# Kernel optimization log

Measured on AMD Instinct MI355X. Metric: run time of the kernel, lower is better.

Reference implementation:

```python
import jax, jax.numpy as jnp
import numpy as np

B, P, F, H, C, D = 512, 32, 16, 4, 32, 128   # graphs, nodes/graph, node feat, heads, head_dim, hidden
N = B * P
E_DIM = 5

def _lin(k, o, i):
    return jax.random.normal(k, (o, i)) * (1.0 / np.sqrt(i))

def setup_inputs():
    key = jax.random.key(0)
    ks = jax.random.split(key, 32)
    # fully-connected directed edges (no self loops) within each graph
    a = np.repeat(np.arange(P), P); b = np.tile(np.arange(P), P)
    m = a != b; a, b = a[m], b[m]
    off = (np.arange(B) * P)[:, None]
    src = (a[None, :] + off).reshape(-1); dst = (b[None, :] + off).reshape(-1)
    edge_index = jnp.asarray(np.stack([src, dst]), dtype=jnp.int32)
    E = src.size
    x = jax.random.normal(ks[0], (N, F))
    edge_attr = jax.random.normal(ks[1], (E, E_DIM))
    z = jnp.zeros
    return dict(
        x=x, edge_index=edge_index, edge_attr=edge_attr,
        W1l=_lin(ks[2], D, F), b1l=z(D), W1r=_lin(ks[3], D, F), b1r=z(D),
        W1e=_lin(ks[4], D, E_DIM), att1=jax.random.normal(ks[5], (1, H, C)) * 0.1, bias1=z(D),
        W2l=_lin(ks[6], D, D), b2l=z(D), W2r=_lin(ks[7], D, D), b2r=z(D),
        W2e=_lin(ks[8], D, E_DIM), att2=jax.random.normal(ks[9], (1, H, C)) * 0.1, bias2=z(D),
        Wc1=_lin(ks[10], D, D), bc1=z(D), Wc2=_lin(ks[11], 1, D), bc2=z(1),
        Ws1=_lin(ks[12], D, D), bs1=z(D), Ws2=_lin(ks[13], 1, D), bs2=z(1),
        Wn1=_lin(ks[14], D, D), bn1=z(D), Wn2=_lin(ks[15], 1, D), bn2=z(1),
    )

def _gatv2(x, src, dst, edge_attr, Wl, bl, Wr, br, We, att, bias):
    # PyG GATv2Conv, concat=True, heads=H, out_channels=C, edge_dim=E_DIM, add_self_loops=False
    E = src.shape[0]
    xl = x @ Wl.T + bl                                   # [N, H*C] messages (source side)
    xr = x @ Wr.T + br                                   # [N, H*C] destination side
    e = (xl[src] + xr[dst] + edge_attr @ We.T).reshape(E, H, C)
    g = jax.nn.leaky_relu(e, 0.2)
    score = jnp.sum(g * att, axis=-1)                    # [E, H]
    smax = jax.ops.segment_max(score, dst, num_segments=N)
    ex = jnp.exp(score - smax[dst])
    denom = jax.ops.segment_sum(ex, dst, num_segments=N)
    alpha = ex / (denom[dst] + 1e-16)                    # segment softmax over in-edges of dst
    msg = xl[src].reshape(E, H, C) * alpha[..., None]
    return jax.ops.segment_sum(msg, dst, num_segments=N).reshape(N, H * C) + bias

def _mlp(h, W1, b1, W2, b2):
    return jax.nn.relu(h @ W1.T + b1) @ W2.T + b2

def reference(x, edge_index, edge_attr, W1l, b1l, W1r, b1r, W1e, att1, bias1,
              W2l, b2l, W2r, b2r, W2e, att2, bias2,
              Wc1, bc1, Wc2, bc2, Ws1, bs1, Ws2, bs2, Wn1, bn1, Wn2, bn2):
    src, dst = edge_index[0], edge_index[1]
    h = _gatv2(x, src, dst, edge_attr, W1l, b1l, W1r, b1r, W1e, att1, bias1)
    hb = h.reshape(B, P, D)
    h = (hb - hb.mean(axis=1, keepdims=True)).reshape(N, D)   # MeanSubtractionNorm per graph
    h = jax.nn.relu(h)
    h = jax.nn.relu(_gatv2(h, src, dst, edge_attr, W2l, b2l, W2r, b2r, W2e, att2, bias2))
    g = h.reshape(B, P, D).mean(axis=1)                       # global_mean_pool (equal-size graphs)
    value = _mlp(g, Wc1, bc1, Wc2, bc2)                       # critic        [B, 1]
    src_logits = _mlp(h, Ws1, bs1, Ws2, bs2).reshape(B, P)    # source_actor, dense per graph
    noop = _mlp(g, Wn1, bn1, Wn2, bn2)                        # noop_actor    [B, 1]
    return jnp.concatenate([value, noop, src_logits], axis=1) # [B, P+2]
```

## Files before the change

kernel.cpp:

```cpp
#include <hip/hip_runtime.h>

#define PP    32
#define FF    16
#define HH    4
#define CC    32
#define DD    128
#define EDIM  5
#define EPG   992
#define NB    512

template <int CTRL>
__device__ __forceinline__ float dpp_add(float v) {
    int t = __builtin_amdgcn_update_dpp(0, __builtin_bit_cast(int, v), CTRL, 0xF, 0xF, true);
    return v + __builtin_bit_cast(float, t);
}
__device__ __forceinline__ float red64(float v) {
    v = dpp_add<0x111>(v);
    v = dpp_add<0x112>(v);
    v = dpp_add<0x114>(v);
    v = dpp_add<0x118>(v);
    v = dpp_add<0x142>(v);
    v = dpp_add<0x143>(v);
    return v;
}
__device__ __forceinline__ float redquad(float v) {
    v = dpp_add<0xB1>(v);
    v = dpp_add<0x4E>(v);
    return v;
}

__device__ __forceinline__ void attention(const float* __restrict__ eattr,
                                          const float* __restrict__ We, const float* __restrict__ att,
                                          const float* __restrict__ bias,
                                          const float* __restrict__ sMsg, const float* __restrict__ sDst,
                                          float* __restrict__ sS, float* __restrict__ sOut,
                                          int tid, long eBase, bool relu)
{
    {
        const int s  = tid >> 4;
        const int ch0 = (tid & 15) * 8;
        float we[40], at[8], xl[8];
#pragma unroll
        for (int q = 0; q < 10; ++q)
            *(float4*)(we + q * 4) = *(const float4*)(We + ch0 * EDIM + q * 4);
        *(float4*)(at)     = *(const float4*)(att + ch0);
        *(float4*)(at + 4) = *(const float4*)(att + ch0 + 4);
        *(float4*)(xl)     = *(const float4*)(sMsg + s * DD + ch0);
        *(float4*)(xl + 4) = *(const float4*)(sMsg + s * DD + ch0 + 4);

        for (int d = 0; d < PP; ++d) {
            int jj = d - (d > s);
            if (jj > 30) jj = 30;
            const float* ea = eattr + (eBase + s * 31 + jj) * EDIM;
            const float e0 = ea[0], e1 = ea[1], e2 = ea[2], e3 = ea[3], e4 = ea[4];
            float xr[8];
            *(float4*)(xr)     = *(const float4*)(sDst + d * DD + ch0);
            *(float4*)(xr + 4) = *(const float4*)(sDst + d * DD + ch0 + 4);
            float acc0 = 0.f, acc1 = 0.f;
#pragma unroll
            for (int c = 0; c < 8; ++c) {
                float v = xl[c] + xr[c];
                const float* w = we + c * EDIM;
                v = fmaf(w[0], e0, v); v = fmaf(w[1], e1, v); v = fmaf(w[2], e2, v);
                v = fmaf(w[3], e3, v); v = fmaf(w[4], e4, v);
                v = fmaf(0.4f, fabsf(v), 0.6f * v);
                if (c & 1) acc1 = fmaf(v, at[c], acc1);
                else       acc0 = fmaf(v, at[c], acc0);
            }
            const float r = redquad(acc0 + acc1);
            if ((tid & 3) == 0)
                sS[s * DD + d * HH + ((tid >> 2) & 3)] = r;
        }
    }
    __syncthreads();
    if (tid < PP * HH) {
        const int d = tid >> 2;
        float mx = -3.4e38f;
#pragma unroll
        for (int s = 0; s < PP; ++s) if (s != d) mx = fmaxf(mx, sS[s * DD + tid]);
        float sum = 0.f;
#pragma unroll
        for (int s = 0; s < PP; ++s) {
            if (s != d) { float ex = __expf(sS[s * DD + tid] - mx); sS[s * DD + tid] = ex; sum += ex; }
        }
        const float inv = 1.f / (sum + 1e-16f);
#pragma unroll
        for (int s = 0; s < PP; ++s)
            sS[s * DD + tid] = (s == d) ? 0.f : sS[s * DD + tid] * inv;
    }
    __syncthreads();
    {
        const int d = tid >> 4, sub = tid & 15;
#pragma unroll
        for (int half = 0; half < 2; ++half) {
            const int ch4 = half * 16 + sub;
            const int idx = d * HH + (ch4 >> 3);
            const float* bp = bias + ch4 * 4;
            float4 acc = make_float4(bp[0], bp[1], bp[2], bp[3]);
#pragma unroll
            for (int s = 0; s < PP; ++s) {
                const float a = sS[s * DD + idx];
                const float4 xv = *(const float4*)(sMsg + s * DD + ch4 * 4);
                acc.x = fmaf(a, xv.x, acc.x);
                acc.y = fmaf(a, xv.y, acc.y);
                acc.z = fmaf(a, xv.z, acc.z);
                acc.w = fmaf(a, xv.w, acc.w);
            }
            if (relu) {
                acc.x = fmaxf(acc.x, 0.f); acc.y = fmaxf(acc.y, 0.f);
                acc.z = fmaxf(acc.z, 0.f); acc.w = fmaxf(acc.w, 0.f);
            }
            *(float4*)(sOut + d * DD + ch4 * 4) = acc;
        }
    }
}

extern "C" __global__ void __launch_bounds__(512, 4)
planetwars_gnn_kernel(const float* __restrict__ x, const float* __restrict__ eattr,
                      const float* __restrict__ W1l, const float* __restrict__ b1l,
                      const float* __restrict__ W1r, const float* __restrict__ b1r,
                      const float* __restrict__ W1e, const float* __restrict__ att1, const float* __restrict__ bias1,
                      const float* __restrict__ W2l, const float* __restrict__ b2l,
                      const float* __restrict__ W2r, const float* __restrict__ b2r,
                      const float* __restrict__ W2e, const float* __restrict__ att2, const float* __restrict__ bias2,
                      const float* __restrict__ Wc1, const float* __restrict__ bc1,
                      const float* __restrict__ Wc2, const float* __restrict__ bc2,
                      const float* __restrict__ Ws1, const float* __restrict__ bs1,
                      const float* __restrict__ Ws2, const float* __restrict__ bs2,
                      const float* __restrict__ Wn1, const float* __restrict__ bn1,
                      const float* __restrict__ Wn2, const float* __restrict__ bn2,
                      float* __restrict__ out)
{
    __shared__ __align__(16) float sA[PP * DD];
    __shared__ __align__(16) float sB[PP * DD];
    __shared__ __align__(16) float sH[PP * DD];
    __shared__ __align__(16) float sU[PP * DD];

    const int tid = threadIdx.x;
    const int g = blockIdx.x;
    const long eBase = (long)g * EPG;

    sU[tid] = x[g * PP * FF + tid];
    __syncthreads();

    {
        const int j = tid & 127, d0 = (tid >> 7) * 8;
        float wl[16], wr[16];
#pragma unroll
        for (int q = 0; q < 4; ++q) {
            *(float4*)(wl + q * 4) = *(const float4*)(W1l + j * FF + q * 4);
            *(float4*)(wr + q * 4) = *(const float4*)(W1r + j * FF + q * 4);
        }
        const float bl = b1l[j], br = b1r[j];
#pragma unroll
        for (int i = 0; i < 8; ++i) {
            const float* xr = sU + (d0 + i) * FF;
            float al = bl, ar = br;
#pragma unroll
            for (int k = 0; k < FF; ++k) {
                const float xv = xr[k];
                al = fmaf(wl[k], xv, al);
                ar = fmaf(wr[k], xv, ar);
            }
            sA[(d0 + i) * DD + j] = al;
            sB[(d0 + i) * DD + j] = ar;
        }
    }
    __syncthreads();

    attention(eattr, W1e, att1, bias1, sA, sB, sU, sH, tid, eBase, false);
    __syncthreads();

    if (tid < DD) {
        float s = 0.f;
#pragma unroll
        for (int d = 0; d < PP; ++d) s += sH[d * DD + tid];
        const float mn = s * (1.0f / 32.0f);
#pragma unroll
        for (int d = 0; d < PP; ++d)
            sH[d * DD + tid] = fmaxf(sH[d * DD + tid] - mn, 0.f);
    }
    __syncthreads();

    {
        const int jj = tid & 63, d0 = (tid >> 6) * 4;
        float accL0[4], accL1[4], accR0[4], accR1[4];
        const float bl0 = b2l[jj], bl1 = b2l[jj + 64];
        const float br0 = b2r[jj], br1 = b2r[jj + 64];
#pragma unroll
        for (int i = 0; i < 4; ++i) { accL0[i] = bl0; accL1[i] = bl1; accR0[i] = br0; accR1[i] = br1; }
        const float* WL0 = W2l + jj * DD;
        const float* WL1 = W2l + (jj + 64) * DD;
        const float* WR0 = W2r + jj * DD;
        const float* WR1 = W2r + (jj + 64) * DD;
        for (int k8 = 0; k8 < 16; ++k8) {
            const float4 l00 = *(const float4*)(WL0 + k8 * 8), l01 = *(const float4*)(WL0 + k8 * 8 + 4);
            const float4 l10 = *(const float4*)(WL1 + k8 * 8), l11 = *(const float4*)(WL1 + k8 * 8 + 4);
            const float4 r00 = *(const float4*)(WR0 + k8 * 8), r01 = *(const float4*)(WR0 + k8 * 8 + 4);
            const float4 r10 = *(const float4*)(WR1 + k8 * 8), r11 = *(const float4*)(WR1 + k8 * 8 + 4);
#pragma unroll
            for (int i = 0; i < 4; ++i) {
                const float4 a0 = *(const float4*)(sH + (d0 + i) * DD + k8 * 8);
                const float4 a1 = *(const float4*)(sH + (d0 + i) * DD + k8 * 8 + 4);
                accL0[i] = fmaf(l00.x, a0.x, accL0[i]); accL0[i] = fmaf(l00.y, a0.y, accL0[i]);
                accL0[i] = fmaf(l00.z, a0.z, accL0[i]); accL0[i] = fmaf(l00.w, a0.w, accL0[i]);
                accL0[i] = fmaf(l01.x, a1.x, accL0[i]); accL0[i] = fmaf(l01.y, a1.y, accL0[i]);
                accL0[i] = fmaf(l01.z, a1.z, accL0[i]); accL0[i] = fmaf(l01.w, a1.w, accL0[i]);
                accL1[i] = fmaf(l10.x, a0.x, accL1[i]); accL1[i] = fmaf(l10.y, a0.y, accL1[i]);
                accL1[i] = fmaf(l10.z, a0.z, accL1[i]); accL1[i] = fmaf(l10.w, a0.w, accL1[i]);
                accL1[i] = fmaf(l11.x, a1.x, accL1[i]); accL1[i] = fmaf(l11.y, a1.y, accL1[i]);
                accL1[i] = fmaf(l11.z, a1.z, accL1[i]); accL1[i] = fmaf(l11.w, a1.w, accL1[i]);
                accR0[i] = fmaf(r00.x, a0.x, accR0[i]); accR0[i] = fmaf(r00.y, a0.y, accR0[i]);
                accR0[i] = fmaf(r00.z, a0.z, accR0[i]); accR0[i] = fmaf(r00.w, a0.w, accR0[i]);
                accR0[i] = fmaf(r01.x, a1.x, accR0[i]); accR0[i] = fmaf(r01.y, a1.y, accR0[i]);
                accR0[i] = fmaf(r01.z, a1.z, accR0[i]); accR0[i] = fmaf(r01.w, a1.w, accR0[i]);
                accR1[i] = fmaf(r10.x, a0.x, accR1[i]); accR1[i] = fmaf(r10.y, a0.y, accR1[i]);
                accR1[i] = fmaf(r10.z, a0.z, accR1[i]); accR1[i] = fmaf(r10.w, a0.w, accR1[i]);
                accR1[i] = fmaf(r11.x, a1.x, accR1[i]); accR1[i] = fmaf(r11.y, a1.y, accR1[i]);
                accR1[i] = fmaf(r11.z, a1.z, accR1[i]); accR1[i] = fmaf(r11.w, a1.w, accR1[i]);
            }
        }
#pragma unroll
        for (int i = 0; i < 4; ++i) {
            sA[(d0 + i) * DD + jj]      = accL0[i];
            sA[(d0 + i) * DD + jj + 64] = accL1[i];
            sB[(d0 + i) * DD + jj]      = accR0[i];
            sB[(d0 + i) * DD + jj + 64] = accR1[i];
        }
    }
    __syncthreads();

    attention(eattr, W2e, att2, bias2, sA, sB, sU, sH, tid, eBase, true);
    __syncthreads();

    if (tid < DD) {
        float s = 0.f;
#pragma unroll
        for (int d = 0; d < PP; ++d) s += sH[d * DD + tid];
        sU[tid] = s * (1.0f / 32.0f);
    }
    __syncthreads();

    {
        const int jj = tid & 63, d0 = (tid >> 6) * 4;
        const float b0 = bs1[jj], b1 = bs1[jj + 64];
        float acc0[4], acc1[4];
#pragma unroll
        for (int i = 0; i < 4; ++i) { acc0[i] = b0; acc1[i] = b1; }
        const float* W0 = Ws1 + jj * DD;
        const float* W1 = Ws1 + (jj + 64) * DD;
        for (int k8 = 0; k8 < 16; ++k8) {
            const float4 w00 = *(const float4*)(W0 + k8 * 8), w01 = *(const float4*)(W0 + k8 * 8 + 4);
            const float4 w10 = *(const float4*)(W1 + k8 * 8), w11 = *(const float4*)(W1 + k8 * 8 + 4);
#pragma unroll
            for (int i = 0; i < 4; ++i) {
                const float4 a0 = *(const float4*)(sH + (d0 + i) * DD + k8 * 8);
                const float4 a1 = *(const float4*)(sH + (d0 + i) * DD + k8 * 8 + 4);
                acc0[i] = fmaf(w00.x, a0.x, acc0[i]); acc0[i] = fmaf(w00.y, a0.y, acc0[i]);
                acc0[i] = fmaf(w00.z, a0.z, acc0[i]); acc0[i] = fmaf(w00.w, a0.w, acc0[i]);
                acc0[i] = fmaf(w01.x, a1.x, acc0[i]); acc0[i] = fmaf(w01.y, a1.y, acc0[i]);
                acc0[i] = fmaf(w01.z, a1.z, acc0[i]); acc0[i] = fmaf(w01.w, a1.w, acc0[i]);
                acc1[i] = fmaf(w10.x, a0.x, acc1[i]); acc1[i] = fmaf(w10.y, a0.y, acc1[i]);
                acc1[i] = fmaf(w10.z, a0.z, acc1[i]); acc1[i] = fmaf(w10.w, a0.w, acc1[i]);
                acc1[i] = fmaf(w11.x, a1.x, acc1[i]); acc1[i] = fmaf(w11.y, a1.y, acc1[i]);
                acc1[i] = fmaf(w11.z, a1.z, acc1[i]); acc1[i] = fmaf(w11.w, a1.w, acc1[i]);
            }
        }
        const float ws2a = Ws2[jj], ws2b = Ws2[jj + 64];
        const float bias2s = bs2[0];
#pragma unroll
        for (int i = 0; i < 4; ++i) {
            const float t = fmaf(fmaxf(acc0[i], 0.f), ws2a, fmaxf(acc1[i], 0.f) * ws2b);
            const float r = red64(t);
            if ((tid & 63) == 63) out[g * 34 + 2 + d0 + i] = r + bias2s;
        }
    }

    if (tid < 128) {
        const int w = tid >> 6, j = tid & 63;
        const float* Wa = (w ? Wn1 : Wc1);
        const float* ba = (w ? bn1 : bc1);
        const float* Wb = (w ? Wn2 : Wc2);
        const float  bb = (w ? bn2 : bc2)[0];
        float h0 = ba[j], h1 = ba[j + 64];
        const float* R0 = Wa + j * DD;
        const float* R1 = Wa + (j + 64) * DD;
#pragma unroll
        for (int k8 = 0; k8 < 16; ++k8) {
            const float4 g0 = *(const float4*)(sU + k8 * 8);
            const float4 g1 = *(const float4*)(sU + k8 * 8 + 4);
            const float4 p00 = *(const float4*)(R0 + k8 * 8), p01 = *(const float4*)(R0 + k8 * 8 + 4);
            const float4 p10 = *(const float4*)(R1 + k8 * 8), p11 = *(const float4*)(R1 + k8 * 8 + 4);
            h0 = fmaf(p00.x, g0.x, h0); h0 = fmaf(p00.y, g0.y, h0);
            h0 = fmaf(p00.z, g0.z, h0); h0 = fmaf(p00.w, g0.w, h0);
            h0 = fmaf(p01.x, g1.x, h0); h0 = fmaf(p01.y, g1.y, h0);
            h0 = fmaf(p01.z, g1.z, h0); h0 = fmaf(p01.w, g1.w, h0);
            h1 = fmaf(p10.x, g0.x, h1); h1 = fmaf(p10.y, g0.y, h1);
            h1 = fmaf(p10.z, g0.z, h1); h1 = fmaf(p10.w, g0.w, h1);
            h1 = fmaf(p11.x, g1.x, h1); h1 = fmaf(p11.y, g1.y, h1);
            h1 = fmaf(p11.z, g1.z, h1); h1 = fmaf(p11.w, g1.w, h1);
        }
        const float t = fmaf(fmaxf(h0, 0.f), Wb[j], fmaxf(h1, 0.f) * Wb[j + 64]);
        const float r = red64(t);
        if (j == 63) out[g * 34 + w] = r + bb;
    }
}

extern "C" void kernel_launch(void* const* d_in, const int* in_sizes, int n_in,
                              void* d_out, int out_size, void* d_ws, size_t ws_size,
                              hipStream_t stream)
{
    (void)in_sizes; (void)n_in; (void)d_ws; (void)ws_size; (void)out_size;
    planetwars_gnn_kernel<<<dim3(NB), dim3(512), 0, stream>>>(
        (const float*)d_in[0], (const float*)d_in[2],
        (const float*)d_in[3], (const float*)d_in[4], (const float*)d_in[5], (const float*)d_in[6],
        (const float*)d_in[7], (const float*)d_in[8], (const float*)d_in[9],
        (const float*)d_in[10], (const float*)d_in[11], (const float*)d_in[12], (const float*)d_in[13],
        (const float*)d_in[14], (const float*)d_in[15], (const float*)d_in[16],
        (const float*)d_in[17], (const float*)d_in[18], (const float*)d_in[19], (const float*)d_in[20],
        (const float*)d_in[21], (const float*)d_in[22], (const float*)d_in[23], (const float*)d_in[24],
        (const float*)d_in[25], (const float*)d_in[26], (const float*)d_in[27], (const float*)d_in[28],
        (float*)d_out);
}
```

Baseline: 252.5 us.

## Double block size to 1024 threads and halve per-thread work in all stages

```diff
diff --git a/kernel.cpp b/kernel.cpp
--- a/kernel.cpp
+++ b/kernel.cpp
@@ -23,9 +23,10 @@
     v = dpp_add<0x143>(v);
     return v;
 }
-__device__ __forceinline__ float redquad(float v) {
-    v = dpp_add<0xB1>(v);
-    v = dpp_add<0x4E>(v);
+__device__ __forceinline__ float red8(float v) {
+    v = dpp_add<0x111>(v);
+    v = dpp_add<0x112>(v);
+    v = dpp_add<0x114>(v);
     return v;
 }
 
@@ -37,39 +38,58 @@
                                           int tid, long eBase, bool relu)
 {
     {
-        const int s  = tid >> 4;
-        const int ch0 = (tid & 15) * 8;
-        float we[40], at[8], xl[8];
-#pragma unroll
-        for (int q = 0; q < 10; ++q)
-            *(float4*)(we + q * 4) = *(const float4*)(We + ch0 * EDIM + q * 4);
-        *(float4*)(at)     = *(const float4*)(att + ch0);
-        *(float4*)(at + 4) = *(const float4*)(att + ch0 + 4);
-        *(float4*)(xl)     = *(const float4*)(sMsg + s * DD + ch0);
-        *(float4*)(xl + 4) = *(const float4*)(sMsg + s * DD + ch0 + 4);
+        const int s = tid >> 5;
+        const int q = tid & 31;
+        float we[4][EDIM], at[4], xl[4];
+        {
+            const float* wp = We + q * 20;
+#pragma unroll
+            for (int c = 0; c < 4; ++c)
+#pragma unroll
+                for (int k = 0; k < EDIM; ++k) we[c][k] = wp[c * EDIM + k];
+        }
+        *(float4*)at = *(const float4*)(att + q * 4);
+        *(float4*)xl = *(const float4*)(sMsg + s * DD + q * 4);
+        const float* eaBase = eattr + (eBase + (long)s * 31) * EDIM;
 
         for (int d = 0; d < PP; ++d) {
             int jj = d - (d > s);
             if (jj > 30) jj = 30;
-            const float* ea = eattr + (eBase + s * 31 + jj) * EDIM;
+            const float* ea = eaBase + jj * EDIM;
             const float e0 = ea[0], e1 = ea[1], e2 = ea[2], e3 = ea[3], e4 = ea[4];
-            float xr[8];
-            *(float4*)(xr)     = *(const float4*)(sDst + d * DD + ch0);
-            *(float4*)(xr + 4) = *(const float4*)(sDst + d * DD + ch0 + 4);
-            float acc0 = 0.f, acc1 = 0.f;
-#pragma unroll
-            for (int c = 0; c < 8; ++c) {
-                float v = xl[c] + xr[c];
-                const float* w = we + c * EDIM;
-                v = fmaf(w[0], e0, v); v = fmaf(w[1], e1, v); v = fmaf(w[2], e2, v);
-                v = fmaf(w[3], e3, v); v = fmaf(w[4], e4, v);
+            const float4 xr = *(const float4*)(sDst + d * DD + q * 4);
+            float acc;
+            {
+                float v = xl[0] + xr.x;
+                v = fmaf(we[0][0], e0, v); v = fmaf(we[0][1], e1, v); v = fmaf(we[0][2], e2, v);
+                v = fmaf(we[0][3], e3, v); v = fmaf(we[0][4], e4, v);
                 v = fmaf(0.4f, fabsf(v), 0.6f * v);
-                if (c & 1) acc1 = fmaf(v, at[c], acc1);
-                else       acc0 = fmaf(v, at[c], acc0);
-            }
-            const float r = redquad(acc0 + acc1);
-            if ((tid & 3) == 0)
-                sS[s * DD + d * HH + ((tid >> 2) & 3)] = r;
+                acc = v * at[0];
+            }
+            {
+                float v = xl[1] + xr.y;
+                v = fmaf(we[1][0], e0, v); v = fmaf(we[1][1], e1, v); v = fmaf(we[1][2], e2, v);
+                v = fmaf(we[1][3], e3, v); v = fmaf(we[1][4], e4, v);
+                v = fmaf(0.4f, fabsf(v), 0.6f * v);
+                acc = fmaf(v, at[1], acc);
+            }
+            {
+                float v = xl[2] + xr.z;
+                v = fmaf(we[2][0], e0, v); v = fmaf(we[2][1], e1, v); v = fmaf(we[2][2], e2, v);
+                v = fmaf(we[2][3], e3, v); v = fmaf(we[2][4], e4, v);
+                v = fmaf(0.4f, fabsf(v), 0.6f * v);
+                acc = fmaf(v, at[2], acc);
+            }
+            {
+                float v = xl[3] + xr.w;
+                v = fmaf(we[3][0], e0, v); v = fmaf(we[3][1], e1, v); v = fmaf(we[3][2], e2, v);
+                v = fmaf(we[3][3], e3, v); v = fmaf(we[3][4], e4, v);
+                v = fmaf(0.4f, fabsf(v), 0.6f * v);
+                acc = fmaf(v, at[3], acc);
+            }
+            const float r = red8(acc);
+            if ((q & 7) == 7)
+                sS[s * DD + d * HH + (q >> 3)] = r;
         }
     }
     __syncthreads();
@@ -90,32 +110,28 @@
     }
     __syncthreads();
     {
-        const int d = tid >> 4, sub = tid & 15;
-#pragma unroll
-        for (int half = 0; half < 2; ++half) {
-            const int ch4 = half * 16 + sub;
-            const int idx = d * HH + (ch4 >> 3);
-            const float* bp = bias + ch4 * 4;
-            float4 acc = make_float4(bp[0], bp[1], bp[2], bp[3]);
-#pragma unroll
-            for (int s = 0; s < PP; ++s) {
-                const float a = sS[s * DD + idx];
-                const float4 xv = *(const float4*)(sMsg + s * DD + ch4 * 4);
-                acc.x = fmaf(a, xv.x, acc.x);
-                acc.y = fmaf(a, xv.y, acc.y);
-                acc.z = fmaf(a, xv.z, acc.z);
-                acc.w = fmaf(a, xv.w, acc.w);
-            }
-            if (relu) {
-                acc.x = fmaxf(acc.x, 0.f); acc.y = fmaxf(acc.y, 0.f);
-                acc.z = fmaxf(acc.z, 0.f); acc.w = fmaxf(acc.w, 0.f);
-            }
-            *(float4*)(sOut + d * DD + ch4 * 4) = acc;
-        }
-    }
-}
-
-extern "C" __global__ void __launch_bounds__(512, 4)
+        const int d = tid >> 5, sub = tid & 31;
+        const int idx = d * HH + (sub >> 3);
+        const float* bp = bias + sub * 4;
+        float4 acc = make_float4(bp[0], bp[1], bp[2], bp[3]);
+#pragma unroll
+        for (int s = 0; s < PP; ++s) {
+            const float a = sS[s * DD + idx];
+            const float4 xv = *(const float4*)(sMsg + s * DD + sub * 4);
+            acc.x = fmaf(a, xv.x, acc.x);
+            acc.y = fmaf(a, xv.y, acc.y);
+            acc.z = fmaf(a, xv.z, acc.z);
+            acc.w = fmaf(a, xv.w, acc.w);
+        }
+        if (relu) {
+            acc.x = fmaxf(acc.x, 0.f); acc.y = fmaxf(acc.y, 0.f);
+            acc.z = fmaxf(acc.z, 0.f); acc.w = fmaxf(acc.w, 0.f);
+        }
+        *(float4*)(sOut + d * DD + sub * 4) = acc;
+    }
+}
+
+extern "C" __global__ void __launch_bounds__(1024, 8)
 planetwars_gnn_kernel(const float* __restrict__ x, const float* __restrict__ eattr,
                       const float* __restrict__ W1l, const float* __restrict__ b1l,
                       const float* __restrict__ W1r, const float* __restrict__ b1r,
@@ -140,20 +156,20 @@
     const int g = blockIdx.x;
     const long eBase = (long)g * EPG;
 
-    sU[tid] = x[g * PP * FF + tid];
-    __syncthreads();
-
-    {
-        const int j = tid & 127, d0 = (tid >> 7) * 8;
+    if (tid < PP * FF) sU[tid] = x[g * PP * FF + tid];
+    __syncthreads();
+
+    {
+        const int j = tid & 127, d0 = (tid >> 7) * 4;
         float wl[16], wr[16];
 #pragma unroll
-        for (int q = 0; q < 4; ++q) {
-            *(float4*)(wl + q * 4) = *(const float4*)(W1l + j * FF + q * 4);
-            *(float4*)(wr + q * 4) = *(const float4*)(W1r + j * FF + q * 4);
+        for (int qq = 0; qq < 4; ++qq) {
+            *(float4*)(wl + qq * 4) = *(const float4*)(W1l + j * FF + qq * 4);
+            *(float4*)(wr + qq * 4) = *(const float4*)(W1r + j * FF + qq * 4);
         }
         const float bl = b1l[j], br = b1r[j];
 #pragma unroll
-        for (int i = 0; i < 8; ++i) {
+        for (int i = 0; i < 4; ++i) {
             const float* xr = sU + (d0 + i) * FF;
             float al = bl, ar = br;
 #pragma unroll
@@ -183,49 +199,34 @@
     __syncthreads();
 
     {
-        const int jj = tid & 63, d0 = (tid >> 6) * 4;
-        float accL0[4], accL1[4], accR0[4], accR1[4];
-        const float bl0 = b2l[jj], bl1 = b2l[jj + 64];
-        const float br0 = b2r[jj], br1 = b2r[jj + 64];
-#pragma unroll
-        for (int i = 0; i < 4; ++i) { accL0[i] = bl0; accL1[i] = bl1; accR0[i] = br0; accR1[i] = br1; }
-        const float* WL0 = W2l + jj * DD;
-        const float* WL1 = W2l + (jj + 64) * DD;
-        const float* WR0 = W2r + jj * DD;
-        const float* WR1 = W2r + (jj + 64) * DD;
+        const int j = tid & 127, d0 = (tid >> 7) * 4;
+        float accL[4], accR[4];
+        const float bl = b2l[j], br = b2r[j];
+#pragma unroll
+        for (int i = 0; i < 4; ++i) { accL[i] = bl; accR[i] = br; }
+        const float* WL = W2l + j * DD;
+        const float* WR = W2r + j * DD;
         for (int k8 = 0; k8 < 16; ++k8) {
-            const float4 l00 = *(const float4*)(WL0 + k8 * 8), l01 = *(const float4*)(WL0 + k8 * 8 + 4);
-            const float4 l10 = *(const float4*)(WL1 + k8 * 8), l11 = *(const float4*)(WL1 + k8 * 8 + 4);
-            const float4 r00 = *(const float4*)(WR0 + k8 * 8), r01 = *(const float4*)(WR0 + k8 * 8 + 4);
-            const float4 r10 = *(const float4*)(WR1 + k8 * 8), r11 = *(const float4*)(WR1 + k8 * 8 + 4);
+            const float4 l0 = *(const float4*)(WL + k8 * 8), l1 = *(const float4*)(WL + k8 * 8 + 4);
+            const float4 r0 = *(const float4*)(WR + k8 * 8), r1 = *(const float4*)(WR + k8 * 8 + 4);
 #pragma unroll
             for (int i = 0; i < 4; ++i) {
                 const float4 a0 = *(const float4*)(sH + (d0 + i) * DD + k8 * 8);
                 const float4 a1 = *(const float4*)(sH + (d0 + i) * DD + k8 * 8 + 4);
-                accL0[i] = fmaf(l00.x, a0.x, accL0[i]); accL0[i] = fmaf(l00.y, a0.y, accL0[i]);
-                accL0[i] = fmaf(l00.z, a0.z, accL0[i]); accL0[i] = fmaf(l00.w, a0.w, accL0[i]);
-                accL0[i] = fmaf(l01.x, a1.x, accL0[i]); accL0[i] = fmaf(l01.y, a1.y, accL0[i]);
-                accL0[i] = fmaf(l01.z, a1.z, accL0[i]); accL0[i] = fmaf(l01.w, a1.w, accL0[i]);
-                accL1[i] = fmaf(l10.x, a0.x, accL1[i]); accL1[i] = fmaf(l10.y, a0.y, accL1[i]);
-                accL1[i] = fmaf(l10.z, a0.z, accL1[i]); accL1[i] = fmaf(l10.w, a0.w, accL1[i]);
-                accL1[i] = fmaf(l11.x, a1.x, accL1[i]); accL1[i] = fmaf(l11.y, a1.y, accL1[i]);
-                accL1[i] = fmaf(l11.z, a1.z, accL1[i]); accL1[i] = fmaf(l11.w, a1.w, accL1[i]);
-                accR0[i] = fmaf(r00.x, a0.x, accR0[i]); accR0[i] = fmaf(r00.y, a0.y, accR0[i]);
-                accR0[i] = fmaf(r00.z, a0.z, accR0[i]); accR0[i] = fmaf(r00.w, a0.w, accR0[i]);
-                accR0[i] = fmaf(r01.x, a1.x, accR0[i]); accR0[i] = fmaf(r01.y, a1.y, accR0[i]);
-                accR0[i] = fmaf(r01.z, a1.z, accR0[i]); accR0[i] = fmaf(r01.w, a1.w, accR0[i]);
-                accR1[i] = fmaf(r10.x, a0.x, accR1[i]); accR1[i] = fmaf(r10.y, a0.y, accR1[i]);
-                accR1[i] = fmaf(r10.z, a0.z, accR1[i]); accR1[i] = fmaf(r10.w, a0.w, accR1[i]);
-                accR1[i] = fmaf(r11.x, a1.x, accR1[i]); accR1[i] = fmaf(r11.y, a1.y, accR1[i]);
-                accR1[i] = fmaf(r11.z, a1.z, accR1[i]); accR1[i] = fmaf(r11.w, a1.w, accR1[i]);
+                accL[i] = fmaf(l0.x, a0.x, accL[i]); accL[i] = fmaf(l0.y, a0.y, accL[i]);
+                accL[i] = fmaf(l0.z, a0.z, accL[i]); accL[i] = fmaf(l0.w, a0.w, accL[i]);
+                accL[i] = fmaf(l1.x, a1.x, accL[i]); accL[i] = fmaf(l1.y, a1.y, accL[i]);
+                accL[i] = fmaf(l1.z, a1.z, accL[i]); accL[i] = fmaf(l1.w, a1.w, accL[i]);
+                accR[i] = fmaf(r0.x, a0.x, accR[i]); accR[i] = fmaf(r0.y, a0.y, accR[i]);
+                accR[i] = fmaf(r0.z, a0.z, accR[i]); accR[i] = fmaf(r0.w, a0.w, accR[i]);
+                accR[i] = fmaf(r1.x, a1.x, accR[i]); accR[i] = fmaf(r1.y, a1.y, accR[i]);
+                accR[i] = fmaf(r1.z, a1.z, accR[i]); accR[i] = fmaf(r1.w, a1.w, accR[i]);
             }
         }
 #pragma unroll
         for (int i = 0; i < 4; ++i) {
-            sA[(d0 + i) * DD + jj]      = accL0[i];
-            sA[(d0 + i) * DD + jj + 64] = accL1[i];
-            sB[(d0 + i) * DD + jj]      = accR0[i];
-            sB[(d0 + i) * DD + jj + 64] = accR1[i];
+            sA[(d0 + i) * DD + j] = accL[i];
+            sB[(d0 + i) * DD + j] = accR[i];
         }
     }
     __syncthreads();
@@ -242,18 +243,18 @@
     __syncthreads();
 
     {
-        const int jj = tid & 63, d0 = (tid >> 6) * 4;
+        const int jj = tid & 63, d0 = (tid >> 6) * 2;
         const float b0 = bs1[jj], b1 = bs1[jj + 64];
-        float acc0[4], acc1[4];
-#pragma unroll
-        for (int i = 0; i < 4; ++i) { acc0[i] = b0; acc1[i] = b1; }
+        float acc0[2], acc1[2];
+#pragma unroll
+        for (int i = 0; i < 2; ++i) { acc0[i] = b0; acc1[i] = b1; }
         const float* W0 = Ws1 + jj * DD;
         const float* W1 = Ws1 + (jj + 64) * DD;
         for (int k8 = 0; k8 < 16; ++k8) {
             const float4 w00 = *(const float4*)(W0 + k8 * 8), w01 = *(const float4*)(W0 + k8 * 8 + 4);
             const float4 w10 = *(const float4*)(W1 + k8 * 8), w11 = *(const float4*)(W1 + k8 * 8 + 4);
 #pragma unroll
-            for (int i = 0; i < 4; ++i) {
+            for (int i = 0; i < 2; ++i) {
                 const float4 a0 = *(const float4*)(sH + (d0 + i) * DD + k8 * 8);
                 const float4 a1 = *(const float4*)(sH + (d0 + i) * DD + k8 * 8 + 4);
                 acc0[i] = fmaf(w00.x, a0.x, acc0[i]); acc0[i] = fmaf(w00.y, a0.y, acc0[i]);
@@ -269,7 +270,7 @@
         const float ws2a = Ws2[jj], ws2b = Ws2[jj + 64];
         const float bias2s = bs2[0];
 #pragma unroll
-        for (int i = 0; i < 4; ++i) {
+        for (int i = 0; i < 2; ++i) {
             const float t = fmaf(fmaxf(acc0[i], 0.f), ws2a, fmaxf(acc1[i], 0.f) * ws2b);
             const float r = red64(t);
             if ((tid & 63) == 63) out[g * 34 + 2 + d0 + i] = r + bias2s;
@@ -311,7 +312,7 @@
                               hipStream_t stream)
 {
     (void)in_sizes; (void)n_in; (void)d_ws; (void)ws_size; (void)out_size;
-    planetwars_gnn_kernel<<<dim3(NB), dim3(512), 0, stream>>>(
+    planetwars_gnn_kernel<<<dim3(NB), dim3(1024), 0, stream>>>(
         (const float*)d_in[0], (const float*)d_in[2],
         (const float*)d_in[3], (const float*)d_in[4], (const float*)d_in[5], (const float*)d_in[6],
         (const float*)d_in[7], (const float*)d_in[8], (const float*)d_in[9],
```

Result: slower. 651.5 us (+158.0%).
